# Kernel tuning notes

Measured on AMD Instinct MI355X. Metric: run time of the kernel, lower is better.

Reference implementation:

```python
import jax, jax.numpy as jnp
import numpy as np

B, C, N, K = 4, 64, 8192, 16
OUT = 128

def setup_inputs() -> dict:
    key = jax.random.key(0)
    k1, k2, k3, k4 = jax.random.split(key, 4)
    x = jax.random.normal(k1, (B, C, N, 1), dtype=jnp.float32)
    edge_index = jax.random.randint(k2, (2, B, N, K), 0, N)
    # BasicConv([2C, OUT]) is a 1x1 Conv2d -> weight [OUT, 2C], bias [OUT]
    W_nn = jax.random.normal(k3, (OUT, 2 * C), dtype=jnp.float32) * 0.02
    b_nn = jax.random.normal(k4, (OUT,), dtype=jnp.float32) * 0.02
    return {"x": x, "edge_index": edge_index, "W_nn": W_nn, "b_nn": b_nn}

def _gather_nodes(x2, idx):
    # x2: [B, C, N], idx: [B, N, K] -> [B, C, N, K]
    return jax.vmap(lambda xb, ib: xb[:, ib])(x2, idx)

def reference(x, edge_index, W_nn, b_nn):
    b, c, n, _ = x.shape
    x2 = x[:, :, :, 0]                      # [B, C, N]
    x_i = _gather_nodes(x2, edge_index[1])  # [B, C, N, K]
    x_j = _gather_nodes(x2, edge_index[0])  # [B, C, N, K]
    x_j = jnp.max(x_j - x_i, axis=-1, keepdims=True)  # [B, C, N, 1]
    # interleave channels: cat([x.unsqueeze(2), x_j.unsqueeze(2)], dim=2).reshape(b, 2c, n, 1)
    h = jnp.concatenate([x[:, :, None], x_j[:, :, None]], axis=2).reshape(b, 2 * c, n, 1)
    # BasicConv: 1x1 conv + bias + ReLU
    out = jnp.einsum('oc,bcn->bon', W_nn, h[:, :, :, 0]) + b_nn[None, :, None]
    return jax.nn.relu(out)[:, :, :, None]  # [B, OUT, N, 1]
```

## Files before the change

### kernel.cpp

```cpp
#include <hip/hip_runtime.h>
#include <cstddef>

#define BB 4
#define CC 64
#define NN 8192
#define KK 16
#define OO 128

#define SW 136
#define SH 136

typedef __attribute__((ext_vector_type(8))) short bf16x8;
typedef __attribute__((ext_vector_type(4))) float f32x4;

__device__ __forceinline__ unsigned short f2b(float f) {
    unsigned u = __builtin_bit_cast(unsigned, f);
    unsigned r = (u + 0x7fffu + ((u >> 16) & 1u)) >> 16;
    return (unsigned short)r;
}

__device__ __forceinline__ float bclo(unsigned d) {
    return __builtin_bit_cast(float, d << 16);
}
__device__ __forceinline__ float bchi(unsigned d) {
    return __builtin_bit_cast(float, d & 0xffff0000u);
}

__global__ __launch_bounds__(256) void transpose_kernel(
        const float* __restrict__ x, unsigned short* __restrict__ xt,
        const float* __restrict__ W, unsigned short* __restrict__ Wbf) {
    __shared__ float tile[64][65];
    const int b  = blockIdx.y;
    const int n0 = blockIdx.x * 64;
    const int t  = threadIdx.x;
    const int ln = t & 63;
    const int r  = t >> 6;

    const float* xb = x + (size_t)b * CC * NN;
    #pragma unroll
    for (int s = 0; s < 64; s += 4) {
        int c = s + r;
        tile[c][ln] = xb[(size_t)c * NN + n0 + ln];
    }
    __syncthreads();
    unsigned short* xtb = xt + ((size_t)b * NN + n0) * CC;
    #pragma unroll
    for (int s = 0; s < 64; s += 4) {
        int n = s + r;
        xtb[n * CC + ln] = f2b(tile[ln][n]);
    }

    if (b == 0 && blockIdx.x < 16) {
        int idx = blockIdx.x * 1024 + t * 4;
        float4 v = *reinterpret_cast<const float4*>(W + idx);
        ushort4 o;
        o.x = f2b(v.x); o.y = f2b(v.y); o.z = f2b(v.z); o.w = f2b(v.w);
        *reinterpret_cast<ushort4*>(Wbf + idx) = o;
    }
}

__global__ __launch_bounds__(256) void main_kernel(
        const unsigned short* __restrict__ xt,
        const unsigned short* __restrict__ Wbf,
        const int*            __restrict__ eidx,
        const float*          __restrict__ bias,
        float*                __restrict__ out) {
    __shared__ unsigned short Wl[128 * SW];
    __shared__ unsigned short hl[64 * SH];
    __shared__ int eL[2048];

    const int t    = threadIdx.x;
    const int lane = t & 63;
    const int w    = t >> 6;
    const int b    = blockIdx.y;
    const int n_base = blockIdx.x * 64;

    const int* e0 = eidx + ((size_t)b * NN + n_base) * KK;
    const int* e1 = e0 + (size_t)BB * NN * KK;
    *reinterpret_cast<int4*>(&eL[t * 4])        = *reinterpret_cast<const int4*>(e0 + t * 4);
    *reinterpret_cast<int4*>(&eL[1024 + t * 4]) = *reinterpret_cast<const int4*>(e1 + t * 4);

    #pragma unroll
    for (int it = 0; it < 8; it++) {
        int flat = it * 2048 + t * 8;
        int row = flat >> 7, col = flat & 127;
        *reinterpret_cast<int4*>(&Wl[row * SW + col]) =
            *reinterpret_cast<const int4*>(Wbf + flat);
    }
    __syncthreads();

    const unsigned short* xtb = xt + (size_t)b * NN * CC;
    const int g = lane >> 3;
    const int p = lane & 7;

    #pragma unroll
    for (int bt = 0; bt < 2; bt++) {
        const int nl = w * 16 + bt * 8 + g;
        uint4 xr = *reinterpret_cast<const uint4*>(xtb + (size_t)(n_base + nl) * CC + p * 8);

        float m[8];
        #pragma unroll
        for (int j = 0; j < 8; j++) m[j] = -1e30f;

        #pragma unroll
        for (int k = 0; k < KK; k++) {
            int ij = eL[nl * KK + k];
            int ii = eL[1024 + nl * KK + k];
            uint4 xj = *reinterpret_cast<const uint4*>(xtb + (size_t)ij * CC + p * 8);
            uint4 xi = *reinterpret_cast<const uint4*>(xtb + (size_t)ii * CC + p * 8);
            m[0] = fmaxf(m[0], bclo(xj.x) - bclo(xi.x));
            m[1] = fmaxf(m[1], bchi(xj.x) - bchi(xi.x));
            m[2] = fmaxf(m[2], bclo(xj.y) - bclo(xi.y));
            m[3] = fmaxf(m[3], bchi(xj.y) - bchi(xi.y));
            m[4] = fmaxf(m[4], bclo(xj.z) - bclo(xi.z));
            m[5] = fmaxf(m[5], bchi(xj.z) - bchi(xi.z));
            m[6] = fmaxf(m[6], bclo(xj.w) - bclo(xi.w));
            m[7] = fmaxf(m[7], bchi(xj.w) - bchi(xi.w));
        }

        unsigned xs[8];
        xs[0] = xr.x & 0xffffu; xs[1] = xr.x >> 16;
        xs[2] = xr.y & 0xffffu; xs[3] = xr.y >> 16;
        xs[4] = xr.z & 0xffffu; xs[5] = xr.z >> 16;
        xs[6] = xr.w & 0xffffu; xs[7] = xr.w >> 16;
        unsigned od[8];
        #pragma unroll
        for (int j = 0; j < 8; j++)
            od[j] = xs[j] | ((unsigned)f2b(m[j]) << 16);

        unsigned short* dst = &hl[nl * SH + p * 16];
        uint4 lo, hi;
        lo.x = od[0]; lo.y = od[1]; lo.z = od[2]; lo.w = od[3];
        hi.x = od[4]; hi.y = od[5]; hi.z = od[6]; hi.w = od[7];
        *reinterpret_cast<uint4*>(dst)     = lo;
        *reinterpret_cast<uint4*>(dst + 8) = hi;
    }
    __syncthreads();

    const int quad = lane >> 4;
    const int l15  = lane & 15;
    const int o0w  = w * 32;

    bf16x8 afr[2][4];
    #pragma unroll
    for (int ot = 0; ot < 2; ot++)
        #pragma unroll
        for (int ks = 0; ks < 4; ks++) {
            const unsigned short* ap = &Wl[(o0w + ot * 16 + l15) * SW + ks * 32 + quad * 8];
            afr[ot][ks] = *reinterpret_cast<const bf16x8*>(ap);
        }

    #pragma unroll
    for (int nt = 0; nt < 4; nt++) {
        f32x4 acc0 = {0.f, 0.f, 0.f, 0.f};
        f32x4 acc1 = {0.f, 0.f, 0.f, 0.f};
        #pragma unroll
        for (int ks = 0; ks < 4; ks++) {
            const unsigned short* bp = &hl[(nt * 16 + l15) * SH + ks * 32 + quad * 8];
            bf16x8 bfr = *reinterpret_cast<const bf16x8*>(bp);
            acc0 = __builtin_amdgcn_mfma_f32_16x16x32_bf16(afr[0][ks], bfr, acc0, 0, 0, 0);
            acc1 = __builtin_amdgcn_mfma_f32_16x16x32_bf16(afr[1][ks], bfr, acc1, 0, 0, 0);
        }
        int n_g = n_base + nt * 16 + l15;
        #pragma unroll
        for (int r = 0; r < 4; r++) {
            int o_a = o0w + quad * 4 + r;
            int o_b = o0w + 16 + quad * 4 + r;
            float va = acc0[r] + bias[o_a];
            float vb = acc1[r] + bias[o_b];
            out[((size_t)b * OO + o_a) * NN + n_g] = fmaxf(va, 0.f);
            out[((size_t)b * OO + o_b) * NN + n_g] = fmaxf(vb, 0.f);
        }
    }
}

extern "C" void kernel_launch(void* const* d_in, const int* in_sizes, int n_in,
                              void* d_out, int out_size, void* d_ws, size_t ws_size,
                              hipStream_t stream) {
    const float* x    = (const float*)d_in[0];
    const int*   eidx = (const int*)d_in[1];
    const float* W    = (const float*)d_in[2];
    const float* bias = (const float*)d_in[3];
    float* out = (float*)d_out;

    unsigned short* xt  = (unsigned short*)d_ws;
    unsigned short* Wbf = (unsigned short*)((char*)d_ws + 4 * 1024 * 1024);

    dim3 blk(256);
    dim3 grid(NN / 64, BB);
    transpose_kernel<<<grid, blk, 0, stream>>>(x, xt, W, Wbf);
    main_kernel<<<grid, blk, 0, stream>>>(xt, Wbf, eidx, bias, out);
}
```

Baseline: 83.21 us.

## Load weight fragments directly from global, drop LDS weight tile, batch gather loads

Drops the 34KB shared-memory weight staging buffer. Each wave now loads its MFMA A-fragments straight from global (L2-resident) bf16 weights before the first barrier, and launch bounds request 4 blocks per CU. The neighbor gather loop is restructured to issue 4 index reads and 8 row loads before any max/subtract, so more memory requests are in flight. The cost is higher register pressure from holding fragments and batched loads across the gather phase, which could cause spills under the occupancy hint.

```diff
diff --git a/kernel.cpp b/kernel.cpp
--- a/kernel.cpp
+++ b/kernel.cpp
@@ -7,7 +7,6 @@
 #define KK 16
 #define OO 128
 
-#define SW 136
 #define SH 136
 
 typedef __attribute__((ext_vector_type(8))) short bf16x8;
@@ -59,13 +58,12 @@
     }
 }
 
-__global__ __launch_bounds__(256) void main_kernel(
+__global__ __launch_bounds__(256, 4) void main_kernel(
         const unsigned short* __restrict__ xt,
         const unsigned short* __restrict__ Wbf,
         const int*            __restrict__ eidx,
         const float*          __restrict__ bias,
         float*                __restrict__ out) {
-    __shared__ unsigned short Wl[128 * SW];
     __shared__ unsigned short hl[64 * SH];
     __shared__ int eL[2048];
 
@@ -80,13 +78,17 @@
     *reinterpret_cast<int4*>(&eL[t * 4])        = *reinterpret_cast<const int4*>(e0 + t * 4);
     *reinterpret_cast<int4*>(&eL[1024 + t * 4]) = *reinterpret_cast<const int4*>(e1 + t * 4);
 
+    const int quad = lane >> 4;
+    const int l15  = lane & 15;
+    const int o0w  = w * 32;
+    bf16x8 afr[2][4];
     #pragma unroll
-    for (int it = 0; it < 8; it++) {
-        int flat = it * 2048 + t * 8;
-        int row = flat >> 7, col = flat & 127;
-        *reinterpret_cast<int4*>(&Wl[row * SW + col]) =
-            *reinterpret_cast<const int4*>(Wbf + flat);
-    }
+    for (int ot = 0; ot < 2; ot++)
+        #pragma unroll
+        for (int ks = 0; ks < 4; ks++)
+            afr[ot][ks] = *reinterpret_cast<const bf16x8*>(
+                Wbf + (o0w + ot * 16 + l15) * OO + ks * 32 + quad * 8);
+
     __syncthreads();
 
     const unsigned short* xtb = xt + (size_t)b * NN * CC;
@@ -103,19 +105,32 @@
         for (int j = 0; j < 8; j++) m[j] = -1e30f;
 
         #pragma unroll
-        for (int k = 0; k < KK; k++) {
-            int ij = eL[nl * KK + k];
-            int ii = eL[1024 + nl * KK + k];
-            uint4 xj = *reinterpret_cast<const uint4*>(xtb + (size_t)ij * CC + p * 8);
-            uint4 xi = *reinterpret_cast<const uint4*>(xtb + (size_t)ii * CC + p * 8);
-            m[0] = fmaxf(m[0], bclo(xj.x) - bclo(xi.x));
-            m[1] = fmaxf(m[1], bchi(xj.x) - bchi(xi.x));
-            m[2] = fmaxf(m[2], bclo(xj.y) - bclo(xi.y));
-            m[3] = fmaxf(m[3], bchi(xj.y) - bchi(xi.y));
-            m[4] = fmaxf(m[4], bclo(xj.z) - bclo(xi.z));
-            m[5] = fmaxf(m[5], bchi(xj.z) - bchi(xi.z));
-            m[6] = fmaxf(m[6], bclo(xj.w) - bclo(xi.w));
-            m[7] = fmaxf(m[7], bchi(xj.w) - bchi(xi.w));
+        for (int q = 0; q < 4; q++) {
+            int kj[4], ki[4];
+            #pragma unroll
+            for (int k4 = 0; k4 < 4; k4++) {
+                int k = q * 4 + k4;
+                kj[k4] = eL[nl * KK + k];
+                ki[k4] = eL[1024 + nl * KK + k];
+            }
+            uint4 aj[4], ai[4];
+            #pragma unroll
+            for (int k4 = 0; k4 < 4; k4++)
+                aj[k4] = *reinterpret_cast<const uint4*>(xtb + (size_t)kj[k4] * CC + p * 8);
+            #pragma unroll
+            for (int k4 = 0; k4 < 4; k4++)
+                ai[k4] = *reinterpret_cast<const uint4*>(xtb + (size_t)ki[k4] * CC + p * 8);
+            #pragma unroll
+            for (int k4 = 0; k4 < 4; k4++) {
+                m[0] = fmaxf(m[0], bclo(aj[k4].x) - bclo(ai[k4].x));
+                m[1] = fmaxf(m[1], bchi(aj[k4].x) - bchi(ai[k4].x));
+                m[2] = fmaxf(m[2], bclo(aj[k4].y) - bclo(ai[k4].y));
+                m[3] = fmaxf(m[3], bchi(aj[k4].y) - bchi(ai[k4].y));
+                m[4] = fmaxf(m[4], bclo(aj[k4].z) - bclo(ai[k4].z));
+                m[5] = fmaxf(m[5], bchi(aj[k4].z) - bchi(ai[k4].z));
+                m[6] = fmaxf(m[6], bclo(aj[k4].w) - bclo(ai[k4].w));
+                m[7] = fmaxf(m[7], bchi(aj[k4].w) - bchi(ai[k4].w));
+            }
         }
 
         unsigned xs[8];
@@ -123,32 +138,20 @@
         xs[2] = xr.y & 0xffffu; xs[3] = xr.y >> 16;
         xs[4] = xr.z & 0xffffu; xs[5] = xr.z >> 16;
         xs[6] = xr.w & 0xffffu; xs[7] = xr.w >> 16;
-        unsigned od[8];
-        #pragma unroll
-        for (int j = 0; j < 8; j++)
-            od[j] = xs[j] | ((unsigned)f2b(m[j]) << 16);
-
+        uint4 lo, hi;
+        lo.x = xs[0] | ((unsigned)f2b(m[0]) << 16);
+        lo.y = xs[1] | ((unsigned)f2b(m[1]) << 16);
+        lo.z = xs[2] | ((unsigned)f2b(m[2]) << 16);
+        lo.w = xs[3] | ((unsigned)f2b(m[3]) << 16);
+        hi.x = xs[4] | ((unsigned)f2b(m[4]) << 16);
+        hi.y = xs[5] | ((unsigned)f2b(m[5]) << 16);
+        hi.z = xs[6] | ((unsigned)f2b(m[6]) << 16);
+        hi.w = xs[7] | ((unsigned)f2b(m[7]) << 16);
         unsigned short* dst = &hl[nl * SH + p * 16];
-        uint4 lo, hi;
-        lo.x = od[0]; lo.y = od[1]; lo.z = od[2]; lo.w = od[3];
-        hi.x = od[4]; hi.y = od[5]; hi.z = od[6]; hi.w = od[7];
         *reinterpret_cast<uint4*>(dst)     = lo;
         *reinterpret_cast<uint4*>(dst + 8) = hi;
     }
     __syncthreads();
-
-    const int quad = lane >> 4;
-    const int l15  = lane & 15;
-    const int o0w  = w * 32;
-
-    bf16x8 afr[2][4];
-    #pragma unroll
-    for (int ot = 0; ot < 2; ot++)
-        #pragma unroll
-        for (int ks = 0; ks < 4; ks++) {
-            const unsigned short* ap = &Wl[(o0w + ot * 16 + l15) * SW + ks * 32 + quad * 8];
-            afr[ot][ks] = *reinterpret_cast<const bf16x8*>(ap);
-        }
 
     #pragma unroll
     for (int nt = 0; nt < 4; nt++) {
```

New measurement: 83.61 us. About the same (+0.5%).
